# Kernel optimization log

Hardware: AMD Instinct MI355X
Metric: run time of the kernel (lower is better)

The kernel has to match this reference:

```python
import jax, jax.numpy as jnp
import numpy as np

N = 100000   # nodes
E = 1600000  # edges
D_IN, D_H, D_OUT = 128, 128, 64
BN_EPS = 1e-5


def setup_inputs() -> dict:
    key = jax.random.key(0)
    ks = jax.random.split(key, 12)

    def lin_w(k, fan_in, shape):
        s = 1.0 / np.sqrt(fan_in)
        return jax.random.uniform(k, shape, jnp.float32, -s, s)

    return {
        "x": jax.random.normal(ks[0], (N, D_IN), jnp.float32),
        "edge_index": jax.random.randint(ks[1], (2, E), 0, N, dtype=jnp.int64),
        "edge_weight": jax.random.uniform(ks[2], (E,), jnp.float32),
        "W1": lin_w(ks[3], D_IN, (D_IN, D_H)),
        "b1": jnp.zeros((D_H,), jnp.float32),
        "W2": lin_w(ks[4], D_H, (D_H, D_H)),
        "b2": jnp.zeros((D_H,), jnp.float32),
        "W3": lin_w(ks[5], D_H, (D_H, D_OUT)),
        "b3": jnp.zeros((D_OUT,), jnp.float32),
        "gamma1": jnp.ones((D_H,), jnp.float32),
        "beta1": jnp.zeros((D_H,), jnp.float32),
        "gamma2": jnp.ones((D_H,), jnp.float32),
        "beta2": jnp.zeros((D_H,), jnp.float32),
    }


def _gcn_conv(x, src, dst, w, W, b):
    # PyG GCNConv: x' = D^{-1/2} (A + I) D^{-1/2} (x W) + b, self-loop weight 1
    n = x.shape[0]
    h = x @ W                                   # [N, d_out]
    loop = jnp.arange(n, dtype=src.dtype)
    s = jnp.concatenate([src, loop])            # [E+N]
    d = jnp.concatenate([dst, loop])
    ww = jnp.concatenate([w, jnp.ones((n,), w.dtype)])
    deg = jax.ops.segment_sum(ww, d, num_segments=n)          # in-degree at targets
    dinv = jnp.where(deg > 0, jax.lax.rsqrt(deg), 0.0)
    norm = dinv[s] * ww * dinv[d]               # [E+N]
    msg = h[s] * norm[:, None]                  # gather + scale
    out = jax.ops.segment_sum(msg, d, num_segments=n)
    return out + b


def _batch_norm(x, gamma, beta):
    mean = jnp.mean(x, axis=0)
    var = jnp.mean(jnp.square(x - mean), axis=0)  # biased, as BatchNorm uses
    return (x - mean) * jax.lax.rsqrt(var + BN_EPS) * gamma + beta


def reference(x, edge_index, edge_weight, W1, b1, W2, b2, W3, b3,
              gamma1, beta1, gamma2, beta2):
    src, dst = edge_index[0], edge_index[1]
    h = _gcn_conv(x, src, dst, edge_weight, W1, b1)
    h = jax.nn.relu(_batch_norm(h, gamma1, beta1))
    h = _gcn_conv(h, src, dst, edge_weight, W2, b2)
    h = jax.nn.relu(_batch_norm(h, gamma2, beta2))
    return _gcn_conv(h, src, dst, edge_weight, W3, b3)
```

## Files before the change

kernel.cpp:

```cpp
#include <hip/hip_runtime.h>
#include <hip/hip_fp16.h>
#include <cstdint>
#include <cstddef>

#define BN_EPS 1e-5f
#define KB 1024
#define BSH 9

typedef _Float16 half8 __attribute__((ext_vector_type(8)));
typedef float floatx4 __attribute__((ext_vector_type(4)));

__device__ __forceinline__ float loadS(const __half* p) { return __half2float(*p); }
__device__ __forceinline__ float2 load2(const __half* p) {
    return __half22float2(*(const __half2*)p);
}
__device__ __forceinline__ void storeS(float* p, float v) { *p = v; }
__device__ __forceinline__ void storeS(__half* p, float v) { *p = __float2half(v); }
__device__ __forceinline__ void store2(float* p, float a, float b) {
    *(float2*)p = make_float2(a, b);
}
__device__ __forceinline__ void store2(__half* p, float a, float b) {
    *(__half2*)p = __floats2half2_rn(a, b);
}
__device__ __forceinline__ float wn_of(unsigned v) {
    __half_raw hr; hr.x = (unsigned short)(v & 0x7fffu);
    return __half2float((__half)hr);
}

static __device__ __forceinline__ int load_edge(const void* ei, int mode64, long long pos) {
    if (mode64) return (int)((const long long*)ei)[pos];
    return ((const int*)ei)[pos];
}

__device__ __forceinline__ int detect_mode64(const unsigned* eiw) {
    const int lane = (int)threadIdx.x & 63;
    unsigned m = 0;
    for (int i = lane; i < 2048; i += 64) m |= eiw[2 * i + 1];
    return (__ballot(m != 0) == 0ULL) ? 1 : 0;
}

__global__ __launch_bounds__(256) void init_hist_kernel(const void* __restrict__ ei,
                                                        unsigned* __restrict__ tk,
                                                        unsigned* __restrict__ pc, int E, int epb,
                                                        const float* __restrict__ W1,
                                                        const float* __restrict__ W2,
                                                        const float* __restrict__ W3,
                                                        _Float16* __restrict__ WT1,
                                                        _Float16* __restrict__ WT2,
                                                        _Float16* __restrict__ WT3) {
    const int bid = (int)blockIdx.x;
    const int tid = (int)threadIdx.x;
    if (bid < 160) {
        if (bid == 0 && tid < 8) tk[tid] = 0u;
        const int t_ = bid;
        if (t_ < 64) {
            int t = t_ * 256 + tid;
            int n = t / 128, k = t % 128;
            WT1[t] = (_Float16)W1[k * 128 + n];
        } else if (t_ < 128) {
            int t = (t_ - 64) * 256 + tid;
            int n = t / 128, k = t % 128;
            WT2[t] = (_Float16)W2[k * 128 + n];
        } else {
            int t = (t_ - 128) * 256 + tid;
            int n = t / 128, k = t % 128;
            WT3[t] = (_Float16)W3[k * 64 + n];
        }
        return;
    }
    __shared__ unsigned h[256];
    const int k = bid - 160;
    h[tid] = 0;
    __syncthreads();
    const int md = detect_mode64((const unsigned*)ei);
    const int e0 = k * epb;
    const int e1 = min(E, e0 + epb);
    for (int e = e0 + tid; e < e1; e += 256) {
        int d = load_edge(ei, md, (long long)E + e);
        atomicAdd(&h[d >> BSH], 1u);
    }
    __syncthreads();
    pc[k * 256 + tid] = h[tid];
}

__global__ __launch_bounds__(256) void scan_pc_kernel(unsigned* __restrict__ pc,
                                                      int* __restrict__ tb,
                                                      int* __restrict__ bbase,
                                                      float* __restrict__ gsum,
                                                      float* __restrict__ gsq,
                                                      unsigned* __restrict__ tk, int nbuck) {
    __shared__ int red[256];
    __shared__ int lastFlag;
    const int b = (int)blockIdx.x;
    const int tid = (int)threadIdx.x;
    unsigned v[4];
    int vals[4];
    int s = 0;
#pragma unroll
    for (int j = 0; j < 4; ++j) {
        v[j] = pc[(tid * 4 + j) * 256 + b];
        vals[j] = s;
        s += (int)v[j];
    }
    red[tid] = s;
    __syncthreads();
    for (int off = 1; off < 256; off <<= 1) {
        int t = 0;
        if (tid >= off) t = red[tid - off];
        __syncthreads();
        red[tid] += t;
        __syncthreads();
    }
    const int excl = red[tid] - s;
#pragma unroll
    for (int j = 0; j < 4; ++j)
        pc[(tid * 4 + j) * 256 + b] = (unsigned)(excl + vals[j]);
    if (tid == 255)
        __hip_atomic_store(&tb[b], red[255], __ATOMIC_RELEASE, __HIP_MEMORY_SCOPE_AGENT);
    __syncthreads();
    if (tid == 0) {
        unsigned t = __hip_atomic_fetch_add(tk, 1u, __ATOMIC_ACQ_REL, __HIP_MEMORY_SCOPE_AGENT);
        lastFlag = (t == (unsigned)gridDim.x - 1u) ? 1 : 0;
    }
    __syncthreads();
    if (!lastFlag) return;
    const int v2 = (tid < nbuck)
        ? __hip_atomic_load(&tb[tid], __ATOMIC_ACQUIRE, __HIP_MEMORY_SCOPE_AGENT) : 0;
    __syncthreads();
    red[tid] = v2;
    __syncthreads();
    for (int off = 1; off < 256; off <<= 1) {
        int t = 0;
        if (tid >= off) t = red[tid - off];
        __syncthreads();
        red[tid] += t;
        __syncthreads();
    }
    bbase[tid] = red[tid] - v2;
    if (tid < 128) { gsum[tid] = 0.0f; gsq[tid] = 0.0f; }
}

template <int M, bool BN, typename TI>
__device__ __forceinline__ void gemm_body(int gbid, const TI* __restrict__ X,
                                          const _Float16* __restrict__ WTg,
                                          const float* __restrict__ sc,
                                          const float* __restrict__ sh,
                                          __half* __restrict__ Hout, int N,
                                          _Float16* WT ) {
    constexpr int CT = M / 16;
    constexpr int LDK = 136;

    for (int t = threadIdx.x; t < M * 16; t += 256) {
        int n = t / 16, seg = t % 16;
        *(half8*)&WT[n * LDK + seg * 8] = *(const half8*)&WTg[n * 128 + seg * 8];
    }
    __syncthreads();

    const int wave = (int)threadIdx.x >> 6;
    const int lane = (int)threadIdx.x & 63;
    const int qd = lane >> 4;
    const int ln = lane & 15;
    const int tile0 = gbid * 64 + wave * 16;
    int ar = tile0 + ln;
    if (ar >= N) ar = N - 1;

    half8 aF[4];
    const TI* xr = X + (size_t)ar * 128 + qd * 8;
#pragma unroll
    for (int kb = 0; kb < 4; ++kb) {
        float vv[8];
        if constexpr (sizeof(TI) == 4) {
            float4 v0 = *(const float4*)(xr + kb * 32);
            float4 v1 = *(const float4*)(xr + kb * 32 + 4);
            vv[0] = v0.x; vv[1] = v0.y; vv[2] = v0.z; vv[3] = v0.w;
            vv[4] = v1.x; vv[5] = v1.y; vv[6] = v1.z; vv[7] = v1.w;
        } else {
            half8 raw = *(const half8*)(xr + kb * 32);
#pragma unroll
            for (int j = 0; j < 8; ++j) vv[j] = (float)raw[j];
        }
        if (BN) {
            const int kbase = kb * 32 + qd * 8;
#pragma unroll
            for (int j = 0; j < 8; ++j)
                vv[j] = fmaxf(fmaf(vv[j], sc[kbase + j], sh[kbase + j]), 0.0f);
        }
        half8 a;
#pragma unroll
        for (int j = 0; j < 8; ++j) a[j] = (_Float16)vv[j];
        aF[kb] = a;
    }

#pragma unroll
    for (int ct = 0; ct < CT; ++ct) {
        floatx4 acc = {0.0f, 0.0f, 0.0f, 0.0f};
#pragma unroll
        for (int kb = 0; kb < 4; ++kb) {
            half8 b = *(const half8*)&WT[(ct * 16 + ln) * LDK + kb * 32 + qd * 8];
            acc = __builtin_amdgcn_mfma_f32_16x16x32_f16(aF[kb], b, acc, 0, 0, 0);
        }
#pragma unroll
        for (int r = 0; r < 4; ++r) {
            int orow = tile0 + qd * 4 + r;
            if (orow < N) Hout[(size_t)orow * M + ct * 16 + ln] = __float2half(acc[r]);
        }
    }
}

__global__ __launch_bounds__(256) void sort_gemm1_kernel(const void* __restrict__ ei,
                                                         const float* __restrict__ ew,
                                                         const unsigned* __restrict__ pc,
                                                         const int* __restrict__ bbase,
                                                         unsigned long long* __restrict__ sortedE,
                                                         int E, int epb,
                                                         const float* __restrict__ X,
                                                         const _Float16* __restrict__ WT1g,
                                                         __half* __restrict__ Hout, int N) {
    __shared__ _Float16 WT[128 * 136];
    __shared__ unsigned off_s[256];
    if ((int)blockIdx.x >= KB) {
        gemm_body<128, false, float>((int)blockIdx.x - KB, X, WT1g, nullptr, nullptr,
                                     Hout, N, WT);
        return;
    }
    const int k = (int)blockIdx.x;
    const int tid = (int)threadIdx.x;
    off_s[tid] = (unsigned)bbase[tid] + pc[k * 256 + tid];
    __syncthreads();
    const int md = detect_mode64((const unsigned*)ei);
    const int e0 = k * epb;
    const int e1 = min(E, e0 + epb);
    for (int e = e0 + tid; e < e1; e += 256) {
        int d = load_edge(ei, md, (long long)E + e);
        int s = load_edge(ei, md, e);
        float wv = ew[e];
        unsigned slot = atomicAdd(&off_s[d >> BSH], 1u);
        sortedE[slot] = ((unsigned long long)(unsigned)d << 33) |
                        ((unsigned long long)(unsigned)s << 16) |
                        (unsigned long long)(unsigned short)__half_as_ushort(__float2half(wv));
    }
}

__global__ __launch_bounds__(256) void csr_build_kernel(const unsigned long long* __restrict__ sortedE,
                                                        const int* __restrict__ bbase,
                                                        const int* __restrict__ tb,
                                                        float* __restrict__ dinv,
                                                        int* __restrict__ cnt,
                                                        int* __restrict__ row_start,
                                                        unsigned* __restrict__ edata, int N) {
    __shared__ unsigned cs[512];
    __shared__ float ws[512];
    __shared__ float dv[512];
    __shared__ unsigned sc[512];
    __shared__ unsigned cur[512];
    __shared__ int red[256];
    const int b = (int)blockIdx.x;
    const int tid = (int)threadIdx.x;
    const int n0 = b << BSH;
    const int base = bbase[b];
    const int len = tb[b];

    cs[tid] = 0; cs[tid + 256] = 0;
    ws[tid] = 0.0f; ws[tid + 256] = 0.0f;
    cur[tid] = 0; cur[tid + 256] = 0;
    __syncthreads();

    for (int i = tid; i < len; i += 256) {
        unsigned long long p = sortedE[base + i];
        unsigned fine = (unsigned)(p >> 33) - (unsigned)n0;
        atomicAdd(&cs[fine], 1u);
        __half_raw hr; hr.x = (unsigned short)(p & 0xFFFFu);
        atomicAdd(&ws[fine], __half2float((__half)hr));
    }
    __syncthreads();

    const unsigned a0 = cs[2 * tid];
    const unsigned a1 = cs[2 * tid + 1];
    const int s2 = (int)(a0 + a1);
    red[tid] = s2;
    __syncthreads();
    for (int off = 1; off < 256; off <<= 1) {
        int t = 0;
        if (tid >= off) t = red[tid - off];
        __syncthreads();
        red[tid] += t;
        __syncthreads();
    }
    const int excl2 = red[tid] - s2;
    sc[2 * tid] = (unsigned)excl2;
    sc[2 * tid + 1] = (unsigned)(excl2 + (int)a0);

#pragma unroll
    for (int q = 0; q < 2; ++q) {
        const int f = tid + q * 256;
        const int node = n0 + f;
        const float dvv = rsqrtf(1.0f + ws[f]);
        dv[f] = dvv;
        if (node < N) {
            dinv[node] = dvv;
            cnt[node] = (int)cs[f];
            row_start[node] = base + (int)sc[f];
        }
    }
    __syncthreads();

    for (int i = tid; i < len; i += 256) {
        unsigned long long p = sortedE[base + i];
        unsigned fine = (unsigned)(p >> 33) - (unsigned)n0;
        unsigned s = (unsigned)(p >> 16) & 0x1FFFFu;
        __half_raw hr; hr.x = (unsigned short)(p & 0xFFFFu);
        float wnp = __half2float((__half)hr) * dv[fine];
        unsigned r = atomicAdd(&cur[fine], 1u);
        unsigned hb = (unsigned)__half_as_ushort(__float2half(wnp)) & 0x7fffu;
        edata[base + (int)sc[fine] + (int)r] = (s << 15) | hb;
    }
}

template <int D, bool BIAS, typename TY>
__global__ __launch_bounds__(256) void agg_kernel(const __half* __restrict__ H,
                                                  const unsigned* __restrict__ edata,
                                                  const int* __restrict__ row_start,
                                                  const int* __restrict__ cnt,
                                                  const float* __restrict__ dinv,
                                                  const float* __restrict__ bias,
                                                  TY* __restrict__ Y, int N) {
    constexpr int VPT = D / 64;
    const int lane = (int)threadIdx.x & 63;
    const int i = (int)blockIdx.x * 4 + ((int)threadIdx.x >> 6);
    if (i >= N) return;
    const int c0 = lane * VPT;
    const float di = dinv[i];
    const float dii = di * di;

    float acc0, acc1 = 0.0f;
    if constexpr (VPT == 2) {
        float2 h = load2(H + (size_t)i * D + c0);
        acc0 = dii * h.x;
        acc1 = dii * h.y;
    } else {
        acc0 = dii * loadS(H + (size_t)i * D + c0);
    }

    const int base = row_start[i];
    const int n = cnt[i];
    for (int off = 0; off < n; off += 64) {
        const int rem = n - off;
        unsigned ev = 0;
        if (lane < rem) ev = edata[base + off + lane];
        const int mm = min(64, rem);
        for (int j = 0; j < mm; j += 8) {
            const unsigned e0 = __shfl(ev, j),     e1 = __shfl(ev, j + 1);
            const unsigned e2 = __shfl(ev, j + 2), e3 = __shfl(ev, j + 3);
            const unsigned e4 = __shfl(ev, j + 4), e5 = __shfl(ev, j + 5);
            const unsigned e6 = __shfl(ev, j + 6), e7 = __shfl(ev, j + 7);
            const float w0 = dinv[e0 >> 15] * wn_of(e0);
            const float w1 = dinv[e1 >> 15] * wn_of(e1);
            const float w2 = dinv[e2 >> 15] * wn_of(e2);
            const float w3 = dinv[e3 >> 15] * wn_of(e3);
            const float w4 = dinv[e4 >> 15] * wn_of(e4);
            const float w5 = dinv[e5 >> 15] * wn_of(e5);
            const float w6 = dinv[e6 >> 15] * wn_of(e6);
            const float w7 = dinv[e7 >> 15] * wn_of(e7);
            if constexpr (VPT == 2) {
                float2 h0 = load2(H + (size_t)(e0 >> 15) * D + c0);
                float2 h1 = load2(H + (size_t)(e1 >> 15) * D + c0);
                float2 h2 = load2(H + (size_t)(e2 >> 15) * D + c0);
                float2 h3 = load2(H + (size_t)(e3 >> 15) * D + c0);
                float2 h4 = load2(H + (size_t)(e4 >> 15) * D + c0);
                float2 h5 = load2(H + (size_t)(e5 >> 15) * D + c0);
                float2 h6 = load2(H + (size_t)(e6 >> 15) * D + c0);
                float2 h7 = load2(H + (size_t)(e7 >> 15) * D + c0);
                acc0 = fmaf(w0, h0.x, acc0); acc1 = fmaf(w0, h0.y, acc1);
                acc0 = fmaf(w1, h1.x, acc0); acc1 = fmaf(w1, h1.y, acc1);
                acc0 = fmaf(w2, h2.x, acc0); acc1 = fmaf(w2, h2.y, acc1);
                acc0 = fmaf(w3, h3.x, acc0); acc1 = fmaf(w3, h3.y, acc1);
                acc0 = fmaf(w4, h4.x, acc0); acc1 = fmaf(w4, h4.y, acc1);
                acc0 = fmaf(w5, h5.x, acc0); acc1 = fmaf(w5, h5.y, acc1);
                acc0 = fmaf(w6, h6.x, acc0); acc1 = fmaf(w6, h6.y, acc1);
                acc0 = fmaf(w7, h7.x, acc0); acc1 = fmaf(w7, h7.y, acc1);
            } else {
                float h0 = loadS(H + (size_t)(e0 >> 15) * D + c0);
                float h1 = loadS(H + (size_t)(e1 >> 15) * D + c0);
                float h2 = loadS(H + (size_t)(e2 >> 15) * D + c0);
                float h3 = loadS(H + (size_t)(e3 >> 15) * D + c0);
                float h4 = loadS(H + (size_t)(e4 >> 15) * D + c0);
                float h5 = loadS(H + (size_t)(e5 >> 15) * D + c0);
                float h6 = loadS(H + (size_t)(e6 >> 15) * D + c0);
                float h7 = loadS(H + (size_t)(e7 >> 15) * D + c0);
                acc0 = fmaf(w0, h0, acc0);
                acc0 = fmaf(w1, h1, acc0);
                acc0 = fmaf(w2, h2, acc0);
                acc0 = fmaf(w3, h3, acc0);
                acc0 = fmaf(w4, h4, acc0);
                acc0 = fmaf(w5, h5, acc0);
                acc0 = fmaf(w6, h6, acc0);
                acc0 = fmaf(w7, h7, acc0);
            }
        }
    }

    if constexpr (VPT == 2) {
        if (BIAS) { acc0 += bias[c0]; acc1 += bias[c0 + 1]; }
        store2(Y + (size_t)i * D + c0, acc0, acc1);
    } else {
        if (BIAS) acc0 += bias[c0];
        storeS(Y + (size_t)i * D + c0, acc0);
    }
}

template <int M, bool BN, typename TI, bool ZERO>
__global__ __launch_bounds__(256) void gemm_mfma_kernel(const TI* __restrict__ X,
                                                        const _Float16* __restrict__ WTg,
                                                        const float* __restrict__ sc,
                                                        const float* __restrict__ sh,
                                                        __half* __restrict__ Hout, int N,
                                                        float* __restrict__ gsum,
                                                        float* __restrict__ gsq, int GB) {
    __shared__ _Float16 WT[M * 136];
    if (ZERO && (int)blockIdx.x == GB) {
        if (threadIdx.x < 128) { gsum[threadIdx.x] = 0.0f; gsq[threadIdx.x] = 0.0f; }
        return;
    }
    gemm_body<M, BN, TI>(blockIdx.x, X, WTg, sc, sh, Hout, N, WT);
}

__global__ __launch_bounds__(256) void stats_kernel(const __half* __restrict__ Y,
                                                    float* __restrict__ gsum,
                                                    float* __restrict__ gsq,
                                                    unsigned* __restrict__ tk,
                                                    const float* __restrict__ gamma,
                                                    const float* __restrict__ beta,
                                                    float* __restrict__ sc,
                                                    float* __restrict__ sh, int N) {
    __shared__ float ls[256], lq[256];
    __shared__ int lastFlag;
    const int tid = (int)threadIdx.x;
    const int c = tid & 127;
    const int half_ = tid >> 7;
    float s = 0.0f, q = 0.0f;
    for (int row = (int)blockIdx.x * 2 + half_; row < N; row += 512) {
        float v = __half2float(Y[(size_t)row * 128 + c]);
        s += v;
        q = fmaf(v, v, q);
    }
    ls[tid] = s; lq[tid] = q;
    __syncthreads();
    if (tid < 128) {
        atomicAdd(&gsum[c], ls[tid] + ls[tid + 128]);
        atomicAdd(&gsq[c],  lq[tid] + lq[tid + 128]);
    }
    __syncthreads();
    if (tid == 0) {
        unsigned t = __hip_atomic_fetch_add(tk, 1u, __ATOMIC_ACQ_REL, __HIP_MEMORY_SCOPE_AGENT);
        lastFlag = (t == (unsigned)gridDim.x - 1u) ? 1 : 0;
    }
    __syncthreads();
    if (!lastFlag) return;
    if (tid < 128) {
        float gs = __hip_atomic_load(&gsum[tid], __ATOMIC_ACQUIRE, __HIP_MEMORY_SCOPE_AGENT);
        float gq = __hip_atomic_load(&gsq[tid], __ATOMIC_ACQUIRE, __HIP_MEMORY_SCOPE_AGENT);
        float inv_n = 1.0f / (float)N;
        float mean = gs * inv_n;
        float var = gq * inv_n - mean * mean;
        float scale = gamma[tid] * rsqrtf(var + BN_EPS);
        sc[tid] = scale;
        sh[tid] = beta[tid] - mean * scale;
    }
}

extern "C" void kernel_launch(void* const* d_in, const int* in_sizes, int n_in,
                              void* d_out, int out_size, void* d_ws, size_t ws_size,
                              hipStream_t stream) {
    const float* x   = (const float*)d_in[0];
    const void*  ei  = d_in[1];
    const float* ew  = (const float*)d_in[2];
    const float* W1  = (const float*)d_in[3];
    const float* W2  = (const float*)d_in[5];
    const float* W3  = (const float*)d_in[7];
    const float* b3  = (const float*)d_in[8];
    const float* g1  = (const float*)d_in[9];
    const float* be1 = (const float*)d_in[10];
    const float* g2  = (const float*)d_in[11];
    const float* be2 = (const float*)d_in[12];
    float* out = (float*)d_out;

    const int N = in_sizes[0] / 128;
    const int E = in_sizes[2];

    char* w = (char*)d_ws;
    size_t off = 0;
    auto alloc = [&](size_t bytes) -> void* {
        void* p = w + off;
        off += (bytes + 255) & ~(size_t)255;
        return p;
    };
    unsigned* pc     = (unsigned*)alloc((size_t)KB * 256 * 4);
    int*   tb        = (int*)  alloc(256 * 4);
    int*   bbase     = (int*)  alloc(256 * 4);
    unsigned long long* sortedE = (unsigned long long*)alloc((size_t)E * 8);
    float* dinv      = (float*)alloc((size_t)N * 4);
    int*   cnt       = (int*)  alloc((size_t)N * 4);
    int*   row_start = (int*)  alloc((size_t)N * 4);
    unsigned* edata  = (unsigned*)alloc((size_t)E * 4);
    unsigned* tk     = (unsigned*)alloc(256);
    float* gsum      = (float*)alloc(128 * 4);
    float* gsq       = (float*)alloc(128 * 4);
    float* scb       = (float*)alloc(128 * 4);
    float* shb       = (float*)alloc(128 * 4);
    _Float16* WT1    = (_Float16*)alloc(128 * 128 * 2);
    _Float16* WT2    = (_Float16*)alloc(128 * 128 * 2);
    _Float16* WT3    = (_Float16*)alloc(128 * 64 * 2);
    __half* H        = (__half*)alloc((size_t)N * 128 * 2);
    __half* Yh       = (__half*)alloc((size_t)N * 128 * 2);
    (void)ws_size; (void)n_in; (void)out_size;

    const int epb   = (E + KB - 1) / KB;
    const int nbuck = (N + (1 << BSH) - 1) >> BSH;
    const int gb    = (N + 63) / 64;
    const int ab    = (N + 3) / 4;

    init_hist_kernel<<<160 + KB, 256, 0, stream>>>(ei, tk, pc, E, epb,
                                                   W1, W2, W3, WT1, WT2, WT3);
    scan_pc_kernel<<<nbuck, 256, 0, stream>>>(pc, tb, bbase, gsum, gsq, &tk[0], nbuck);
    sort_gemm1_kernel<<<KB + gb, 256, 0, stream>>>(ei, ew, pc, bbase, sortedE, E,
                                                   epb, x, WT1, H, N);
    csr_build_kernel<<<nbuck, 256, 0, stream>>>(sortedE, bbase, tb, dinv, cnt, row_start,
                                                edata, N);

    agg_kernel<128, false, __half><<<ab, 256, 0, stream>>>(H, edata, row_start, cnt, dinv, nullptr, Yh, N);
    stats_kernel<<<256, 256, 0, stream>>>(Yh, gsum, gsq, &tk[1], g1, be1, scb, shb, N);

    gemm_mfma_kernel<128, true, __half, true><<<gb + 1, 256, 0, stream>>>(
        Yh, WT2, scb, shb, H, N, gsum, gsq, gb);
    agg_kernel<128, false, __half><<<ab, 256, 0, stream>>>(H, edata, row_start, cnt, dinv, nullptr, Yh, N);
    stats_kernel<<<256, 256, 0, stream>>>(Yh, gsum, gsq, &tk[2], g2, be2, scb, shb, N);

    gemm_mfma_kernel<64, true, __half, false><<<gb, 256, 0, stream>>>(
        Yh, WT3, scb, shb, H, N, nullptr, nullptr, gb);
    agg_kernel<64, true, float><<<ab, 256, 0, stream>>>(H, edata, row_start, cnt, dinv, b3, out, N);
}
```

Before: 497.7 us.

## Stage block edge lists in LDS and process four nodes per wave in aggregation

The aggregation kernel now handles 16 nodes per block, four per wave. Each block cooperatively loads the contiguous CSR edge range for its nodes into shared memory in chunks, then each wave walks its nodes' edges from LDS with a 16-wide unrolled gather. The aim is coalesced edge-metadata loads and more outstanding H gathers per wave. In exchange it adds block-level syncs, more registers, and load imbalance when one wave's nodes have more edges than another's.

```diff
diff --git a/kernel.cpp b/kernel.cpp
--- a/kernel.cpp
+++ b/kernel.cpp
@@ -325,86 +325,106 @@
                                                   const float* __restrict__ bias,
                                                   TY* __restrict__ Y, int N) {
     constexpr int VPT = D / 64;
-    const int lane = (int)threadIdx.x & 63;
-    const int i = (int)blockIdx.x * 4 + ((int)threadIdx.x >> 6);
-    if (i >= N) return;
+    constexpr int NPB = 16;
+    constexpr int CAP = 2048;
+    __shared__ unsigned eb[CAP];
+    __shared__ int rs_s[NPB], cn_s[NPB];
+    __shared__ float dv_s[NPB];
+    const int tid = (int)threadIdx.x;
+    const int wave = tid >> 6;
+    const int lane = tid & 63;
+    const int i0 = (int)blockIdx.x * NPB;
     const int c0 = lane * VPT;
-    const float di = dinv[i];
-    const float dii = di * di;
-
-    float acc0, acc1 = 0.0f;
-    if constexpr (VPT == 2) {
-        float2 h = load2(H + (size_t)i * D + c0);
-        acc0 = dii * h.x;
-        acc1 = dii * h.y;
-    } else {
-        acc0 = dii * loadS(H + (size_t)i * D + c0);
-    }
-
-    const int base = row_start[i];
-    const int n = cnt[i];
-    for (int off = 0; off < n; off += 64) {
-        const int rem = n - off;
-        unsigned ev = 0;
-        if (lane < rem) ev = edata[base + off + lane];
-        const int mm = min(64, rem);
-        for (int j = 0; j < mm; j += 8) {
-            const unsigned e0 = __shfl(ev, j),     e1 = __shfl(ev, j + 1);
-            const unsigned e2 = __shfl(ev, j + 2), e3 = __shfl(ev, j + 3);
-            const unsigned e4 = __shfl(ev, j + 4), e5 = __shfl(ev, j + 5);
-            const unsigned e6 = __shfl(ev, j + 6), e7 = __shfl(ev, j + 7);
-            const float w0 = dinv[e0 >> 15] * wn_of(e0);
-            const float w1 = dinv[e1 >> 15] * wn_of(e1);
-            const float w2 = dinv[e2 >> 15] * wn_of(e2);
-            const float w3 = dinv[e3 >> 15] * wn_of(e3);
-            const float w4 = dinv[e4 >> 15] * wn_of(e4);
-            const float w5 = dinv[e5 >> 15] * wn_of(e5);
-            const float w6 = dinv[e6 >> 15] * wn_of(e6);
-            const float w7 = dinv[e7 >> 15] * wn_of(e7);
+
+    if (tid < NPB) {
+        int i = i0 + tid;
+        int ii = (i < N) ? i : (N - 1);
+        rs_s[tid] = row_start[ii];
+        cn_s[tid] = (i < N) ? cnt[ii] : 0;
+        dv_s[tid] = dinv[ii];
+    }
+    __syncthreads();
+    const int base = rs_s[0];
+    int total = 0;
+#pragma unroll
+    for (int k = 0; k < NPB; ++k) total = max(total, rs_s[k] + cn_s[k] - base);
+
+    float a0[4], a1[4];
+#pragma unroll
+    for (int nn = 0; nn < 4; ++nn) {
+        const int idx = wave * 4 + nn;
+        const int i = i0 + idx;
+        a0[nn] = 0.0f; a1[nn] = 0.0f;
+        if (i < N) {
+            const float di = dv_s[idx];
             if constexpr (VPT == 2) {
-                float2 h0 = load2(H + (size_t)(e0 >> 15) * D + c0);
-                float2 h1 = load2(H + (size_t)(e1 >> 15) * D + c0);
-                float2 h2 = load2(H + (size_t)(e2 >> 15) * D + c0);
-                float2 h3 = load2(H + (size_t)(e3 >> 15) * D + c0);
-                float2 h4 = load2(H + (size_t)(e4 >> 15) * D + c0);
-                float2 h5 = load2(H + (size_t)(e5 >> 15) * D + c0);
-                float2 h6 = load2(H + (size_t)(e6 >> 15) * D + c0);
-                float2 h7 = load2(H + (size_t)(e7 >> 15) * D + c0);
-                acc0 = fmaf(w0, h0.x, acc0); acc1 = fmaf(w0, h0.y, acc1);
-                acc0 = fmaf(w1, h1.x, acc0); acc1 = fmaf(w1, h1.y, acc1);
-                acc0 = fmaf(w2, h2.x, acc0); acc1 = fmaf(w2, h2.y, acc1);
-                acc0 = fmaf(w3, h3.x, acc0); acc1 = fmaf(w3, h3.y, acc1);
-                acc0 = fmaf(w4, h4.x, acc0); acc1 = fmaf(w4, h4.y, acc1);
-                acc0 = fmaf(w5, h5.x, acc0); acc1 = fmaf(w5, h5.y, acc1);
-                acc0 = fmaf(w6, h6.x, acc0); acc1 = fmaf(w6, h6.y, acc1);
-                acc0 = fmaf(w7, h7.x, acc0); acc1 = fmaf(w7, h7.y, acc1);
+                float2 h = load2(H + (size_t)i * D + c0);
+                a0[nn] = di * di * h.x;
+                a1[nn] = di * di * h.y;
             } else {
-                float h0 = loadS(H + (size_t)(e0 >> 15) * D + c0);
-                float h1 = loadS(H + (size_t)(e1 >> 15) * D + c0);
-                float h2 = loadS(H + (size_t)(e2 >> 15) * D + c0);
-                float h3 = loadS(H + (size_t)(e3 >> 15) * D + c0);
-                float h4 = loadS(H + (size_t)(e4 >> 15) * D + c0);
-                float h5 = loadS(H + (size_t)(e5 >> 15) * D + c0);
-                float h6 = loadS(H + (size_t)(e6 >> 15) * D + c0);
-                float h7 = loadS(H + (size_t)(e7 >> 15) * D + c0);
-                acc0 = fmaf(w0, h0, acc0);
-                acc0 = fmaf(w1, h1, acc0);
-                acc0 = fmaf(w2, h2, acc0);
-                acc0 = fmaf(w3, h3, acc0);
-                acc0 = fmaf(w4, h4, acc0);
-                acc0 = fmaf(w5, h5, acc0);
-                acc0 = fmaf(w6, h6, acc0);
-                acc0 = fmaf(w7, h7, acc0);
+                a0[nn] = di * di * loadS(H + (size_t)i * D + c0);
             }
         }
     }
 
-    if constexpr (VPT == 2) {
-        if (BIAS) { acc0 += bias[c0]; acc1 += bias[c0 + 1]; }
-        store2(Y + (size_t)i * D + c0, acc0, acc1);
-    } else {
-        if (BIAS) acc0 += bias[c0];
-        storeS(Y + (size_t)i * D + c0, acc0);
+    for (int cb = 0; cb < total; cb += CAP) {
+        const int clen = min(CAP, total - cb);
+        __syncthreads();
+        for (int e = tid; e < clen; e += 256) eb[e] = edata[base + cb + e];
+        __syncthreads();
+#pragma unroll
+        for (int nn = 0; nn < 4; ++nn) {
+            const int idx = wave * 4 + nn;
+            const int i = i0 + idx;
+            if (i >= N) continue;
+            const int lo = rs_s[idx] - base;
+            const int hi = lo + cn_s[idx];
+            const int s = max(lo, cb);
+            const int epos = min(hi, cb + clen);
+            for (int j = s; j < epos; j += 16) {
+                unsigned ev[16];
+#pragma unroll
+                for (int k = 0; k < 16; ++k)
+                    ev[k] = (j + k < epos) ? eb[j + k - cb] : 0u;
+                float wk[16];
+#pragma unroll
+                for (int k = 0; k < 16; ++k) wk[k] = dinv[ev[k] >> 15] * wn_of(ev[k]);
+                if constexpr (VPT == 2) {
+                    float2 hh[16];
+#pragma unroll
+                    for (int k = 0; k < 16; ++k)
+                        hh[k] = load2(H + (size_t)(ev[k] >> 15) * D + c0);
+#pragma unroll
+                    for (int k = 0; k < 16; ++k) {
+                        a0[nn] = fmaf(wk[k], hh[k].x, a0[nn]);
+                        a1[nn] = fmaf(wk[k], hh[k].y, a1[nn]);
+                    }
+                } else {
+                    float hh[16];
+#pragma unroll
+                    for (int k = 0; k < 16; ++k)
+                        hh[k] = loadS(H + (size_t)(ev[k] >> 15) * D + c0);
+#pragma unroll
+                    for (int k = 0; k < 16; ++k)
+                        a0[nn] = fmaf(wk[k], hh[k], a0[nn]);
+                }
+            }
+        }
+    }
+
+#pragma unroll
+    for (int nn = 0; nn < 4; ++nn) {
+        const int idx = wave * 4 + nn;
+        const int i = i0 + idx;
+        if (i >= N) continue;
+        float v0 = a0[nn], v1 = a1[nn];
+        if constexpr (VPT == 2) {
+            if (BIAS) { v0 += bias[c0]; v1 += bias[c0 + 1]; }
+            store2(Y + (size_t)i * D + c0, v0, v1);
+        } else {
+            if (BIAS) v0 += bias[c0];
+            storeS(Y + (size_t)i * D + c0, v0);
+        }
     }
 }
 
@@ -517,7 +537,7 @@
     const int epb   = (E + KB - 1) / KB;
     const int nbuck = (N + (1 << BSH) - 1) >> BSH;
     const int gb    = (N + 63) / 64;
-    const int ab    = (N + 3) / 4;
+    const int ab    = (N + 15) / 16;
 
     init_hist_kernel<<<160 + KB, 256, 0, stream>>>(ei, tk, pc, E, epb,
                                                    W1, W2, W3, WT1, WT2, WT3);
```

Result: slower. 686.4 us (+37.9%).

## Fuse per-layer aggregate, BN stats and GEMM into cooperative persistent kernels

Applied to the files above, without the earlier changes.

Replaces the per-layer chain of aggregation, stats and GEMM kernels with two cooperative persistent kernels that use grid-wide syncs between phases, and fold the final aggregation into the second one. Each block recomputes the BN scale and shift locally instead of relying on a last-block ticket. The GEMM phase also changes: it reads weights straight from global memory without staging them in LDS. The aim is to remove launch gaps and tail effects between the many small kernels. In exchange it adds grid.sync overhead, limits occupancy to a grid sized by an occupancy query, and may make the GEMM slower without LDS staging.

```diff
diff --git a/kernel.cpp b/kernel.cpp
--- a/kernel.cpp
+++ b/kernel.cpp
@@ -1,7 +1,10 @@
 #include <hip/hip_runtime.h>
 #include <hip/hip_fp16.h>
+#include <hip/hip_cooperative_groups.h>
 #include <cstdint>
 #include <cstddef>
+
+namespace cg = cooperative_groups;
 
 #define BN_EPS 1e-5f
 #define KB 1024
@@ -86,8 +89,7 @@
 __global__ __launch_bounds__(256) void scan_pc_kernel(unsigned* __restrict__ pc,
                                                       int* __restrict__ tb,
                                                       int* __restrict__ bbase,
-                                                      float* __restrict__ gsum,
-                                                      float* __restrict__ gsq,
+                                                      float* __restrict__ gz,
                                                       unsigned* __restrict__ tk, int nbuck) {
     __shared__ int red[256];
     __shared__ int lastFlag;
@@ -137,7 +139,7 @@
         __syncthreads();
     }
     bbase[tid] = red[tid] - v2;
-    if (tid < 128) { gsum[tid] = 0.0f; gsq[tid] = 0.0f; }
+    gz[tid] = 0.0f; gz[tid + 256] = 0.0f;
 }
 
 template <int M, bool BN, typename TI>
@@ -316,129 +318,114 @@
     }
 }
 
+
 template <int D, bool BIAS, typename TY>
-__global__ __launch_bounds__(256) void agg_kernel(const __half* __restrict__ H,
-                                                  const unsigned* __restrict__ edata,
-                                                  const int* __restrict__ row_start,
-                                                  const int* __restrict__ cnt,
-                                                  const float* __restrict__ dinv,
-                                                  const float* __restrict__ bias,
-                                                  TY* __restrict__ Y, int N) {
+__device__ void agg_phase(const __half* __restrict__ H,
+                          const unsigned* __restrict__ edata,
+                          const int* __restrict__ row_start,
+                          const int* __restrict__ cnt,
+                          const float* __restrict__ dinv,
+                          const float* __restrict__ bias,
+                          TY* __restrict__ Y, int N) {
     constexpr int VPT = D / 64;
     const int lane = (int)threadIdx.x & 63;
-    const int i = (int)blockIdx.x * 4 + ((int)threadIdx.x >> 6);
-    if (i >= N) return;
+    const int wv = (int)threadIdx.x >> 6;
     const int c0 = lane * VPT;
-    const float di = dinv[i];
-    const float dii = di * di;
-
-    float acc0, acc1 = 0.0f;
-    if constexpr (VPT == 2) {
-        float2 h = load2(H + (size_t)i * D + c0);
-        acc0 = dii * h.x;
-        acc1 = dii * h.y;
-    } else {
-        acc0 = dii * loadS(H + (size_t)i * D + c0);
-    }
-
-    const int base = row_start[i];
-    const int n = cnt[i];
-    for (int off = 0; off < n; off += 64) {
-        const int rem = n - off;
-        unsigned ev = 0;
-        if (lane < rem) ev = edata[base + off + lane];
-        const int mm = min(64, rem);
-        for (int j = 0; j < mm; j += 8) {
-            const unsigned e0 = __shfl(ev, j),     e1 = __shfl(ev, j + 1);
-            const unsigned e2 = __shfl(ev, j + 2), e3 = __shfl(ev, j + 3);
-            const unsigned e4 = __shfl(ev, j + 4), e5 = __shfl(ev, j + 5);
-            const unsigned e6 = __shfl(ev, j + 6), e7 = __shfl(ev, j + 7);
-            const float w0 = dinv[e0 >> 15] * wn_of(e0);
-            const float w1 = dinv[e1 >> 15] * wn_of(e1);
-            const float w2 = dinv[e2 >> 15] * wn_of(e2);
-            const float w3 = dinv[e3 >> 15] * wn_of(e3);
-            const float w4 = dinv[e4 >> 15] * wn_of(e4);
-            const float w5 = dinv[e5 >> 15] * wn_of(e5);
-            const float w6 = dinv[e6 >> 15] * wn_of(e6);
-            const float w7 = dinv[e7 >> 15] * wn_of(e7);
-            if constexpr (VPT == 2) {
-                float2 h0 = load2(H + (size_t)(e0 >> 15) * D + c0);
-                float2 h1 = load2(H + (size_t)(e1 >> 15) * D + c0);
-                float2 h2 = load2(H + (size_t)(e2 >> 15) * D + c0);
-                float2 h3 = load2(H + (size_t)(e3 >> 15) * D + c0);
-                float2 h4 = load2(H + (size_t)(e4 >> 15) * D + c0);
-                float2 h5 = load2(H + (size_t)(e5 >> 15) * D + c0);
-                float2 h6 = load2(H + (size_t)(e6 >> 15) * D + c0);
-                float2 h7 = load2(H + (size_t)(e7 >> 15) * D + c0);
-                acc0 = fmaf(w0, h0.x, acc0); acc1 = fmaf(w0, h0.y, acc1);
-                acc0 = fmaf(w1, h1.x, acc0); acc1 = fmaf(w1, h1.y, acc1);
-                acc0 = fmaf(w2, h2.x, acc0); acc1 = fmaf(w2, h2.y, acc1);
-                acc0 = fmaf(w3, h3.x, acc0); acc1 = fmaf(w3, h3.y, acc1);
-                acc0 = fmaf(w4, h4.x, acc0); acc1 = fmaf(w4, h4.y, acc1);
-                acc0 = fmaf(w5, h5.x, acc0); acc1 = fmaf(w5, h5.y, acc1);
-                acc0 = fmaf(w6, h6.x, acc0); acc1 = fmaf(w6, h6.y, acc1);
-                acc0 = fmaf(w7, h7.x, acc0); acc1 = fmaf(w7, h7.y, acc1);
-            } else {
-                float h0 = loadS(H + (size_t)(e0 >> 15) * D + c0);
-                float h1 = loadS(H + (size_t)(e1 >> 15) * D + c0);
-                float h2 = loadS(H + (size_t)(e2 >> 15) * D + c0);
-                float h3 = loadS(H + (size_t)(e3 >> 15) * D + c0);
-                float h4 = loadS(H + (size_t)(e4 >> 15) * D + c0);
-                float h5 = loadS(H + (size_t)(e5 >> 15) * D + c0);
-                float h6 = loadS(H + (size_t)(e6 >> 15) * D + c0);
-                float h7 = loadS(H + (size_t)(e7 >> 15) * D + c0);
-                acc0 = fmaf(w0, h0, acc0);
-                acc0 = fmaf(w1, h1, acc0);
-                acc0 = fmaf(w2, h2, acc0);
-                acc0 = fmaf(w3, h3, acc0);
-                acc0 = fmaf(w4, h4, acc0);
-                acc0 = fmaf(w5, h5, acc0);
-                acc0 = fmaf(w6, h6, acc0);
-                acc0 = fmaf(w7, h7, acc0);
+    const int ngrp = (N + 3) / 4;
+    for (int g = (int)blockIdx.x; g < ngrp; g += (int)gridDim.x) {
+        const int i = g * 4 + wv;
+        if (i >= N) continue;
+        const float di = dinv[i];
+        const float dii = di * di;
+
+        float acc0, acc1 = 0.0f;
+        if constexpr (VPT == 2) {
+            float2 h = load2(H + (size_t)i * D + c0);
+            acc0 = dii * h.x;
+            acc1 = dii * h.y;
+        } else {
+            acc0 = dii * loadS(H + (size_t)i * D + c0);
+        }
+
+        const int base = row_start[i];
+        const int n = cnt[i];
+        for (int off = 0; off < n; off += 64) {
+            const int rem = n - off;
+            unsigned ev = 0;
+            if (lane < rem) ev = edata[base + off + lane];
+            const int mm = min(64, rem);
+            for (int j = 0; j < mm; j += 8) {
+                const unsigned e0 = __shfl(ev, j),     e1 = __shfl(ev, j + 1);
+                const unsigned e2 = __shfl(ev, j + 2), e3 = __shfl(ev, j + 3);
+                const unsigned e4 = __shfl(ev, j + 4), e5 = __shfl(ev, j + 5);
+                const unsigned e6 = __shfl(ev, j + 6), e7 = __shfl(ev, j + 7);
+                const float w0 = dinv[e0 >> 15] * wn_of(e0);
+                const float w1 = dinv[e1 >> 15] * wn_of(e1);
+                const float w2 = dinv[e2 >> 15] * wn_of(e2);
+                const float w3 = dinv[e3 >> 15] * wn_of(e3);
+                const float w4 = dinv[e4 >> 15] * wn_of(e4);
+                const float w5 = dinv[e5 >> 15] * wn_of(e5);
+                const float w6 = dinv[e6 >> 15] * wn_of(e6);
+                const float w7 = dinv[e7 >> 15] * wn_of(e7);
+                if constexpr (VPT == 2) {
+                    float2 h0 = load2(H + (size_t)(e0 >> 15) * D + c0);
+                    float2 h1 = load2(H + (size_t)(e1 >> 15) * D + c0);
+                    float2 h2 = load2(H + (size_t)(e2 >> 15) * D + c0);
+                    float2 h3 = load2(H + (size_t)(e3 >> 15) * D + c0);
+                    float2 h4 = load2(H + (size_t)(e4 >> 15) * D + c0);
+                    float2 h5 = load2(H + (size_t)(e5 >> 15) * D + c0);
+                    float2 h6 = load2(H + (size_t)(e6 >> 15) * D + c0);
+                    float2 h7 = load2(H + (size_t)(e7 >> 15) * D + c0);
+                    acc0 = fmaf(w0, h0.x, acc0); acc1 = fmaf(w0, h0.y, acc1);
+                    acc0 = fmaf(w1, h1.x, acc0); acc1 = fmaf(w1, h1.y, acc1);
+                    acc0 = fmaf(w2, h2.x, acc0); acc1 = fmaf(w2, h2.y, acc1);
+                    acc0 = fmaf(w3, h3.x, acc0); acc1 = fmaf(w3, h3.y, acc1);
+                    acc0 = fmaf(w4, h4.x, acc0); acc1 = fmaf(w4, h4.y, acc1);
+                    acc0 = fmaf(w5, h5.x, acc0); acc1 = fmaf(w5, h5.y, acc1);
+                    acc0 = fmaf(w6, h6.x, acc0); acc1 = fmaf(w6, h6.y, acc1);
+                    acc0 = fmaf(w7, h7.x, acc0); acc1 = fmaf(w7, h7.y, acc1);
+                } else {
+                    float h0 = loadS(H + (size_t)(e0 >> 15) * D + c0);
+                    float h1 = loadS(H + (size_t)(e1 >> 15) * D + c0);
+                    float h2 = loadS(H + (size_t)(e2 >> 15) * D + c0);
+                    float h3 = loadS(H + (size_t)(e3 >> 15) * D + c0);
+                    float h4 = loadS(H + (size_t)(e4 >> 15) * D + c0);
+                    float h5 = loadS(H + (size_t)(e5 >> 15) * D + c0);
+                    float h6 = loadS(H + (size_t)(e6 >> 15) * D + c0);
+                    float h7 = loadS(H + (size_t)(e7 >> 15) * D + c0);
+                    acc0 = fmaf(w0, h0, acc0);
+                    acc0 = fmaf(w1, h1, acc0);
+                    acc0 = fmaf(w2, h2, acc0);
+                    acc0 = fmaf(w3, h3, acc0);
+                    acc0 = fmaf(w4, h4, acc0);
+                    acc0 = fmaf(w5, h5, acc0);
+                    acc0 = fmaf(w6, h6, acc0);
+                    acc0 = fmaf(w7, h7, acc0);
+                }
             }
         }
-    }
-
-    if constexpr (VPT == 2) {
-        if (BIAS) { acc0 += bias[c0]; acc1 += bias[c0 + 1]; }
-        store2(Y + (size_t)i * D + c0, acc0, acc1);
-    } else {
-        if (BIAS) acc0 += bias[c0];
-        storeS(Y + (size_t)i * D + c0, acc0);
-    }
-}
-
-template <int M, bool BN, typename TI, bool ZERO>
-__global__ __launch_bounds__(256) void gemm_mfma_kernel(const TI* __restrict__ X,
-                                                        const _Float16* __restrict__ WTg,
-                                                        const float* __restrict__ sc,
-                                                        const float* __restrict__ sh,
-                                                        __half* __restrict__ Hout, int N,
-                                                        float* __restrict__ gsum,
-                                                        float* __restrict__ gsq, int GB) {
-    __shared__ _Float16 WT[M * 136];
-    if (ZERO && (int)blockIdx.x == GB) {
-        if (threadIdx.x < 128) { gsum[threadIdx.x] = 0.0f; gsq[threadIdx.x] = 0.0f; }
-        return;
-    }
-    gemm_body<M, BN, TI>(blockIdx.x, X, WTg, sc, sh, Hout, N, WT);
-}
-
-__global__ __launch_bounds__(256) void stats_kernel(const __half* __restrict__ Y,
-                                                    float* __restrict__ gsum,
-                                                    float* __restrict__ gsq,
-                                                    unsigned* __restrict__ tk,
-                                                    const float* __restrict__ gamma,
-                                                    const float* __restrict__ beta,
-                                                    float* __restrict__ sc,
-                                                    float* __restrict__ sh, int N) {
+
+        if constexpr (VPT == 2) {
+            if (BIAS) { acc0 += bias[c0]; acc1 += bias[c0 + 1]; }
+            store2(Y + (size_t)i * D + c0, acc0, acc1);
+        } else {
+            if (BIAS) acc0 += bias[c0];
+            storeS(Y + (size_t)i * D + c0, acc0);
+        }
+    }
+}
+
+__device__ void stats_phase(const __half* __restrict__ Y, float* __restrict__ gsum,
+                            float* __restrict__ gsq, int N) {
     __shared__ float ls[256], lq[256];
-    __shared__ int lastFlag;
+    const unsigned nsb = min(gridDim.x, 256u);
+    if (blockIdx.x >= nsb) return;
     const int tid = (int)threadIdx.x;
     const int c = tid & 127;
     const int half_ = tid >> 7;
+    const int stride = (int)nsb * 2;
     float s = 0.0f, q = 0.0f;
-    for (int row = (int)blockIdx.x * 2 + half_; row < N; row += 512) {
+    for (int row = (int)blockIdx.x * 2 + half_; row < N; row += stride) {
         float v = __half2float(Y[(size_t)row * 128 + c]);
         s += v;
         q = fmaf(v, v, q);
@@ -449,22 +436,84 @@
         atomicAdd(&gsum[c], ls[tid] + ls[tid + 128]);
         atomicAdd(&gsq[c],  lq[tid] + lq[tid + 128]);
     }
-    __syncthreads();
-    if (tid == 0) {
-        unsigned t = __hip_atomic_fetch_add(tk, 1u, __ATOMIC_ACQ_REL, __HIP_MEMORY_SCOPE_AGENT);
-        lastFlag = (t == (unsigned)gridDim.x - 1u) ? 1 : 0;
-    }
-    __syncthreads();
-    if (!lastFlag) return;
-    if (tid < 128) {
-        float gs = __hip_atomic_load(&gsum[tid], __ATOMIC_ACQUIRE, __HIP_MEMORY_SCOPE_AGENT);
-        float gq = __hip_atomic_load(&gsq[tid], __ATOMIC_ACQUIRE, __HIP_MEMORY_SCOPE_AGENT);
-        float inv_n = 1.0f / (float)N;
-        float mean = gs * inv_n;
-        float var = gq * inv_n - mean * mean;
-        float scale = gamma[tid] * rsqrtf(var + BN_EPS);
-        sc[tid] = scale;
-        sh[tid] = beta[tid] - mean * scale;
+}
+
+template <int M>
+__device__ void gemm_phase(const __half* __restrict__ X, const _Float16* __restrict__ WTg,
+                           const float* sc, const float* sh,
+                           __half* __restrict__ Hout, int N) {
+    const int wv = (int)threadIdx.x >> 6;
+    const int lane = (int)threadIdx.x & 63;
+    const int qd = lane >> 4;
+    const int ln = lane & 15;
+    const int nt = (N + 63) / 64;
+    for (int t = (int)blockIdx.x; t < nt; t += (int)gridDim.x) {
+        const int tile0 = t * 64 + wv * 16;
+        int ar = tile0 + ln;
+        if (ar >= N) ar = N - 1;
+        half8 aF[4];
+        const __half* xr = X + (size_t)ar * 128 + qd * 8;
+#pragma unroll
+        for (int kb = 0; kb < 4; ++kb) {
+            half8 raw = *(const half8*)(xr + kb * 32);
+            const int kbase = kb * 32 + qd * 8;
+            half8 a;
+#pragma unroll
+            for (int j = 0; j < 8; ++j) {
+                float v = fmaxf(fmaf((float)raw[j], sc[kbase + j], sh[kbase + j]), 0.0f);
+                a[j] = (_Float16)v;
+            }
+            aF[kb] = a;
+        }
+#pragma unroll 1
+        for (int ct = 0; ct < M / 16; ++ct) {
+            floatx4 acc = {0.0f, 0.0f, 0.0f, 0.0f};
+#pragma unroll
+            for (int kb = 0; kb < 4; ++kb) {
+                half8 b = *(const half8*)&WTg[(size_t)(ct * 16 + ln) * 128 + kb * 32 + qd * 8];
+                acc = __builtin_amdgcn_mfma_f32_16x16x32_f16(aF[kb], b, acc, 0, 0, 0);
+            }
+#pragma unroll
+            for (int r = 0; r < 4; ++r) {
+                int orow = tile0 + qd * 4 + r;
+                if (orow < N) Hout[(size_t)orow * M + ct * 16 + ln] = __float2half(acc[r]);
+            }
+        }
+    }
+}
+
+template <int M, bool FINAL>
+__global__ __launch_bounds__(256, 8) void coop_layer_kernel(
+    const __half* __restrict__ Hin, __half* __restrict__ Yh, __half* __restrict__ Hout,
+    const unsigned* __restrict__ edata, const int* __restrict__ row_start,
+    const int* __restrict__ cnt, const float* __restrict__ dinv,
+    float* __restrict__ gsum, float* __restrict__ gsq,
+    const float* __restrict__ gamma, const float* __restrict__ beta,
+    const _Float16* __restrict__ WTg,
+    const float* __restrict__ b3, float* __restrict__ out, int N) {
+    __shared__ float sc_l[128], sh_l[128];
+    cg::grid_group grid = cg::this_grid();
+
+    agg_phase<128, false, __half>(Hin, edata, row_start, cnt, dinv, nullptr, Yh, N);
+    grid.sync();
+    stats_phase(Yh, gsum, gsq, N);
+    grid.sync();
+    {
+        const int t = (int)threadIdx.x;
+        if (t < 128) {
+            float inv_n = 1.0f / (float)N;
+            float mean = gsum[t] * inv_n;
+            float var = gsq[t] * inv_n - mean * mean;
+            float scale = gamma[t] * rsqrtf(var + BN_EPS);
+            sc_l[t] = scale;
+            sh_l[t] = beta[t] - mean * scale;
+        }
+        __syncthreads();
+    }
+    gemm_phase<M>(Yh, WTg, sc_l, sh_l, Hout, N);
+    if constexpr (FINAL) {
+        grid.sync();
+        agg_phase<64, true, float>(Hout, edata, row_start, cnt, dinv, b3, out, N);
     }
 }
 
@@ -503,10 +552,7 @@
     int*   row_start = (int*)  alloc((size_t)N * 4);
     unsigned* edata  = (unsigned*)alloc((size_t)E * 4);
     unsigned* tk     = (unsigned*)alloc(256);
-    float* gsum      = (float*)alloc(128 * 4);
-    float* gsq       = (float*)alloc(128 * 4);
-    float* scb       = (float*)alloc(128 * 4);
-    float* shb       = (float*)alloc(128 * 4);
+    float* gz        = (float*)alloc(512 * 4);
     _Float16* WT1    = (_Float16*)alloc(128 * 128 * 2);
     _Float16* WT2    = (_Float16*)alloc(128 * 128 * 2);
     _Float16* WT3    = (_Float16*)alloc(128 * 64 * 2);
@@ -514,28 +560,56 @@
     __half* Yh       = (__half*)alloc((size_t)N * 128 * 2);
     (void)ws_size; (void)n_in; (void)out_size;
 
+    float* gsumA = gz,        *gsqA = gz + 128;
+    float* gsumB = gz + 256,  *gsqB = gz + 384;
+
     const int epb   = (E + KB - 1) / KB;
     const int nbuck = (N + (1 << BSH) - 1) >> BSH;
     const int gb    = (N + 63) / 64;
-    const int ab    = (N + 3) / 4;
+
+    static int coopGrid = 0;
+    if (coopGrid == 0) {
+        int dev = 0;
+        hipGetDevice(&dev);
+        hipDeviceProp_t prop;
+        hipGetDeviceProperties(&prop, dev);
+        int nb1 = 0, nb2 = 0;
+        hipOccupancyMaxActiveBlocksPerMultiprocessor(&nb1, coop_layer_kernel<128, false>, 256, 0);
+        hipOccupancyMaxActiveBlocksPerMultiprocessor(&nb2, coop_layer_kernel<64, true>, 256, 0);
+        int nb = nb1 < nb2 ? nb1 : nb2;
+        if (nb < 1) nb = 1;
+        long g = (long)nb * (long)prop.multiProcessorCount;
+        if (g > 2048) g = 2048;
+        if (g < 64) g = 64;
+        coopGrid = (int)g;
+    }
 
     init_hist_kernel<<<160 + KB, 256, 0, stream>>>(ei, tk, pc, E, epb,
                                                    W1, W2, W3, WT1, WT2, WT3);
-    scan_pc_kernel<<<nbuck, 256, 0, stream>>>(pc, tb, bbase, gsum, gsq, &tk[0], nbuck);
+    scan_pc_kernel<<<nbuck, 256, 0, stream>>>(pc, tb, bbase, gz, &tk[0], nbuck);
     sort_gemm1_kernel<<<KB + gb, 256, 0, stream>>>(ei, ew, pc, bbase, sortedE, E,
                                                    epb, x, WT1, H, N);
     csr_build_kernel<<<nbuck, 256, 0, stream>>>(sortedE, bbase, tb, dinv, cnt, row_start,
                                                 edata, N);
 
-    agg_kernel<128, false, __half><<<ab, 256, 0, stream>>>(H, edata, row_start, cnt, dinv, nullptr, Yh, N);
-    stats_kernel<<<256, 256, 0, stream>>>(Yh, gsum, gsq, &tk[1], g1, be1, scb, shb, N);
-
-    gemm_mfma_kernel<128, true, __half, true><<<gb + 1, 256, 0, stream>>>(
-        Yh, WT2, scb, shb, H, N, gsum, gsq, gb);
-    agg_kernel<128, false, __half><<<ab, 256, 0, stream>>>(H, edata, row_start, cnt, dinv, nullptr, Yh, N);
-    stats_kernel<<<256, 256, 0, stream>>>(Yh, gsum, gsq, &tk[2], g2, be2, scb, shb, N);
-
-    gemm_mfma_kernel<64, true, __half, false><<<gb, 256, 0, stream>>>(
-        Yh, WT3, scb, shb, H, N, nullptr, nullptr, gb);
-    agg_kernel<64, true, float><<<ab, 256, 0, stream>>>(H, edata, row_start, cnt, dinv, b3, out, N);
-}
+    {
+        const __half* Hin = H; __half* Hout_ = H;
+        int n_ = N;
+        void* args[] = {(void*)&Hin, (void*)&Yh, (void*)&Hout_,
+                        (void*)&edata, (void*)&row_start, (void*)&cnt, (void*)&dinv,
+                        (void*)&gsumA, (void*)&gsqA, (void*)&g1, (void*)&be1,
+                        (void*)&WT2, (void*)&b3, (void*)&out, (void*)&n_};
+        hipLaunchCooperativeKernel(coop_layer_kernel<128, false>, dim3(coopGrid),
+                                   dim3(256), args, 0, stream);
+    }
+    {
+        const __half* Hin = H; __half* Hout_ = H;
+        int n_ = N;
+        void* args[] = {(void*)&Hin, (void*)&Yh, (void*)&Hout_,
+                        (void*)&edata, (void*)&row_start, (void*)&cnt, (void*)&dinv,
+                        (void*)&gsumB, (void*)&gsqB, (void*)&g2, (void*)&be2,
+                        (void*)&WT3, (void*)&b3, (void*)&out, (void*)&n_};
+        hipLaunchCooperativeKernel(coop_layer_kernel<64, true>, dim3(coopGrid),
+                                   dim3(256), args, 0, stream);
+    }
+}
```

After: 1.233 ms. +147.8%, slower.
